# Optimization experiments

Measured on AMD Instinct MI355X. Metric: run time of the kernel, lower is better.

Reference implementation:

```python
import jax, jax.numpy as jnp
import numpy as np

B, D, H, NB = 4096, 2048, 2048, 4
BIN, BOUT = D // NB, H // NB
EPS = 1e-5


def _block_linear(x, W, b):
    # x: [B, nb*bin], W: [nb, bin, bout], b: [nb, bout] -> [B, nb*bout]
    xr = x.reshape(x.shape[0], NB, BIN)
    y = jnp.einsum('bni,nio->bno', xr, W) + b
    return y.reshape(x.shape[0], NB * BOUT)


def setup_inputs() -> dict:
    key = jax.random.key(0)
    ks = jax.random.split(key, 24)
    sW = 1.0 / np.sqrt(BIN)
    sR = 1.0 / np.sqrt(BOUT)
    inp = {
        'x': jax.random.normal(ks[0], (B, D), jnp.float32),
        'h_prev': jax.random.normal(ks[1], (B, H), jnp.float32),
        'c_prev': jax.random.normal(ks[2], (B, H), jnp.float32),
        'ln_g': jnp.ones((D,), jnp.float32),
        'ln_b': jnp.zeros((D,), jnp.float32),
        'conv_w': jax.random.normal(ks[3], (3,), jnp.float32) * 0.5,
        'conv_b': jnp.zeros((), jnp.float32),
    }
    names = ['Wz', 'Wi', 'Wf', 'Wo']
    for j, n in enumerate(names):
        inp[n] = jax.random.normal(ks[4 + j], (NB, BIN, BOUT), jnp.float32) * sW
        inp['b' + n[1]] = jax.random.normal(ks[8 + j], (NB, BOUT), jnp.float32) * sW
    rnames = ['Rz', 'Ri', 'Rf', 'Ro']
    for j, n in enumerate(rnames):
        inp[n] = jax.random.normal(ks[12 + j], (NB, BOUT, BOUT), jnp.float32) * sR
        inp['rb' + n[1]] = jax.random.normal(ks[16 + j], (NB, BOUT), jnp.float32) * sR
    return inp


def reference(x, h_prev, c_prev, ln_g, ln_b, conv_w, conv_b,
              Wz, bz, Wi, bi, Wf, bf, Wo, bo,
              Rz, rbz, Ri, rbi, Rf, rbf, Ro, rbo):
    # LayerNorm over the feature dim
    mu = jnp.mean(x, axis=-1, keepdims=True)
    var = jnp.mean((x - mu) ** 2, axis=-1, keepdims=True)
    x_norm = (x - mu) * jax.lax.rsqrt(var + EPS) * ln_g + ln_b

    # Causal conv1d (kernel 3) along the feature axis, then SiLU
    xp = jnp.pad(x_norm, ((0, 0), (2, 0)))  # left-pad 2 -> causal
    xc = conv_w[0] * xp[:, :D] + conv_w[1] * xp[:, 1:D + 1] + conv_w[2] * xp[:, 2:D + 2] + conv_b
    x_conv = jax.nn.silu(xc)

    z = jnp.tanh(_block_linear(x, Wz, bz) + _block_linear(h_prev, Rz, rbz))
    i = jax.nn.sigmoid(_block_linear(x_conv, Wi, bi) + _block_linear(h_prev, Ri, rbi))
    f = jax.nn.sigmoid(_block_linear(x_conv, Wf, bf) + _block_linear(h_prev, Rf, rbf))
    o = jax.nn.sigmoid(_block_linear(x, Wo, bo) + _block_linear(h_prev, Ro, rbo))

    c_t = f * c_prev + i * z
    h_t = o * jnp.tanh(c_t)
    return (h_t, c_t)
```

## Files before the change

kernel.cpp:

```cpp
#include <hip/hip_runtime.h>
#include <hip/hip_bf16.h>
#include <math.h>

#define BB 4096
#define DD 2048
#define HH 2048

typedef __bf16 bf16x8 __attribute__((ext_vector_type(8)));
typedef float f32x4 __attribute__((ext_vector_type(4)));

__device__ __forceinline__ void async16(const void* g, void* l) {
  __builtin_amdgcn_global_load_lds(
      (const __attribute__((address_space(1))) unsigned int*)g,
      (__attribute__((address_space(3))) unsigned int*)l,
      16, 0, 0);
}

__device__ __forceinline__ float sigmoidf_(float x) {
  return 1.0f / (1.0f + __expf(-x));
}
__device__ __forceinline__ float tanhf_(float x) {
  float t = __expf(-2.0f * fabsf(x));
  return copysignf((1.0f - t) / (1.0f + t), x);
}

__device__ __forceinline__ void store_bf8(__hip_bfloat16* dst, const float* v) {
  union { __hip_bfloat16 b[8]; uint4 u; } p;
#pragma unroll
  for (int e = 0; e < 8; e++) p.b[e] = __float2bfloat16(v[e]);
  *(uint4*)dst = p.u;
}

__global__ void prep_bias(const float* __restrict__ bz, const float* __restrict__ bi,
                          const float* __restrict__ bf, const float* __restrict__ bo,
                          const float* __restrict__ rbz, const float* __restrict__ rbi,
                          const float* __restrict__ rbf, const float* __restrict__ rbo,
                          float* __restrict__ bias) {
  int i = blockIdx.x * 256 + threadIdx.x;
  if (i < 2048) {
    bias[0 * 2048 + i] = bz[i] + rbz[i];
    bias[1 * 2048 + i] = bi[i] + rbi[i];
    bias[2 * 2048 + i] = bf[i] + rbf[i];
    bias[3 * 2048 + i] = bo[i] + rbo[i];
  }
}

__global__ __launch_bounds__(256) void prep_w(
    const float* __restrict__ Wz, const float* __restrict__ Wi,
    const float* __restrict__ Wf, const float* __restrict__ Wo,
    const float* __restrict__ Rz, const float* __restrict__ Ri,
    const float* __restrict__ Rf, const float* __restrict__ Ro,
    __hip_bfloat16* __restrict__ WT2) {
  const int jt = blockIdx.x;
  const int ksg = blockIdx.y;
  const int gn = blockIdx.z;
  const int g = gn >> 2, nn = gn & 3;
  const float* src;
  if (ksg < 4) src = (g == 0 ? Wz : g == 1 ? Wi : g == 2 ? Wf : Wo);
  else         src = (g == 0 ? Rz : g == 1 ? Ri : g == 2 ? Rf : Ro);
  const int t = threadIdx.x;
#pragma unroll
  for (int q = 0; q < 2; q++) {
    int u = t + q * 256;
    int ksl = u >> 7, j = (u >> 2) & 31, pc = u & 3;
    int c = pc ^ ((j >> 1) & 3);
    int kr = (ksg & 3) * 128 + ksl * 32 + c * 8;
    const float* s0 = src + ((size_t)nn * 512 + kr) * 512 + jt * 32 + j;
    float v[8];
#pragma unroll
    for (int e = 0; e < 8; e++) v[e] = s0[(size_t)e * 512];
    size_t gr = ((size_t)(gn * 16 + jt) * 32 + ksg * 4 + ksl) * 128 + j * 4 + pc;
    store_bf8(WT2 + gr * 8, v);
  }
}

__global__ __launch_bounds__(256) void prep_act(
    const float* __restrict__ x, const float* __restrict__ h,
    const float* __restrict__ lg, const float* __restrict__ lb,
    const float* __restrict__ cw, const float* __restrict__ cb,
    __hip_bfloat16* __restrict__ xh2, __hip_bfloat16* __restrict__ xc2) {
  const int r = blockIdx.x, t = threadIdx.x, l = t & 63;
  const int mb = r >> 7, rl = r & 127, swz = (rl >> 1) & 3;
  const int n = t >> 6, ktl = (t >> 2) & 15, pc = (t & 3) ^ swz;
  __shared__ float red[8];
  __shared__ float edge[256][2];
  const float* xr = x + (size_t)r * 2048;
  const float* hr = h + (size_t)r * 2048;
  float4 v0 = ((const float4*)xr)[t * 2];
  float4 v1 = ((const float4*)xr)[t * 2 + 1];
  float vv[8] = {v0.x, v0.y, v0.z, v0.w, v1.x, v1.y, v1.z, v1.w};
  float s = 0.f, s2 = 0.f;
#pragma unroll
  for (int e = 0; e < 8; e++) { s += vv[e]; s2 += vv[e] * vv[e]; }
#pragma unroll
  for (int off = 32; off > 0; off >>= 1) {
    s += __shfl_down(s, off);
    s2 += __shfl_down(s2, off);
  }
  const int w = t >> 6;
  if (l == 0) { red[w] = s; red[4 + w] = s2; }
  __syncthreads();
  const float mu = (red[0] + red[1] + red[2] + red[3]) * (1.0f / 2048.0f);
  const float var = (red[4] + red[5] + red[6] + red[7]) * (1.0f / 2048.0f) - mu * mu;
  const float rs = rsqrtf(var + 1e-5f);

  float4 h0 = ((const float4*)hr)[t * 2];
  float4 h1 = ((const float4*)hr)[t * 2 + 1];
  float hh[8] = {h0.x, h0.y, h0.z, h0.w, h1.x, h1.y, h1.z, h1.w};
  float4 g0 = ((const float4*)lg)[t * 2], g1 = ((const float4*)lg)[t * 2 + 1];
  float4 b0 = ((const float4*)lb)[t * 2], b1 = ((const float4*)lb)[t * 2 + 1];
  float gg[8] = {g0.x, g0.y, g0.z, g0.w, g1.x, g1.y, g1.z, g1.w};
  float bb[8] = {b0.x, b0.y, b0.z, b0.w, b1.x, b1.y, b1.z, b1.w};
  float fr[8];
#pragma unroll
  for (int e = 0; e < 8; e++) fr[e] = (vv[e] - mu) * rs * gg[e] + bb[e];

  const size_t bx = ((size_t)(mb * 4 + n) * 32 + ktl) * 512 + rl * 4 + pc;
  const size_t bh = ((size_t)(mb * 4 + n) * 32 + 16 + ktl) * 512 + rl * 4 + pc;
  store_bf8(xh2 + bx * 8, vv);
  store_bf8(xh2 + bh * 8, hh);

  edge[t][0] = fr[6]; edge[t][1] = fr[7];
  __syncthreads();
  float p6 = __shfl_up(fr[6], 1);
  float p7 = __shfl_up(fr[7], 1);
  if (l == 0) {
    p6 = (t > 0) ? edge[t - 1][0] : 0.f;
    p7 = (t > 0) ? edge[t - 1][1] : 0.f;
  }
  const float w0 = cw[0], w1 = cw[1], w2 = cw[2], cbv = cb[0];
  float sc[8];
  {
    float xc0 = w0 * p6 + w1 * p7 + w2 * fr[0] + cbv;
    float xc1 = w0 * p7 + w1 * fr[0] + w2 * fr[1] + cbv;
    sc[0] = xc0 * sigmoidf_(xc0);
    sc[1] = xc1 * sigmoidf_(xc1);
  }
#pragma unroll
  for (int e = 2; e < 8; e++) {
    float xc = w0 * fr[e - 2] + w1 * fr[e - 1] + w2 * fr[e] + cbv;
    sc[e] = xc * sigmoidf_(xc);
  }
  const size_t bc = ((size_t)(mb * 4 + n) * 16 + ktl) * 512 + rl * 4 + pc;
  store_bf8(xc2 + bc * 8, sc);
}

__global__ __launch_bounds__(512, 4) void gemm_fused(
    const __hip_bfloat16* __restrict__ xh2, const __hip_bfloat16* __restrict__ xc2,
    const __hip_bfloat16* __restrict__ WT2, const float* __restrict__ bias,
    const float* __restrict__ c_prev, float* __restrict__ out) {
  __shared__ __attribute__((aligned(16))) char smem[65536];
  __hip_bfloat16* zo = (__hip_bfloat16*)smem;

  const int mb = blockIdx.x, jt = blockIdx.y, n = blockIdx.z;
  const int t = threadIdx.x, w = t >> 6, l = t & 63;
  const int pair = w >> 2, mhalf = (w >> 1) & 1, jhalf = w & 1;
  const int lj = l & 15;

  const char* pA = (const char*)xh2 + (size_t)(mb * 4 + n) * 262144 + t * 16;
  const char* pC = (const char*)xc2 + (size_t)(mb * 4 + n) * 131072 + t * 16;
  const char* pB = (const char*)WT2 +
      (size_t)(n * 16 + jt * 2 + ((t >> 8) & 1)) * 65536 + ((t >> 7) & 1) * 2048 + (t & 127) * 16;
  char* dA = smem + t * 16;
  char* dB = smem + 32768 + t * 16;

  const int fo = lj * 64 + (((l >> 4) ^ ((lj >> 1) & 3)) * 16);
  const int g0 = pair ? 1 : 0, g1 = pair ? 2 : 3;

  f32x4 acc[4][2][2] = {};

  for (int ks2 = 0; ks2 < 16; ++ks2) {
    __syncthreads();
    async16(pA, dA);
    async16(pA + 8192, dA + 8192);
    if (ks2 < 8) {
      async16(pC, dA + 16384);
      async16(pC + 8192, dA + 24576);
    }
    async16(pB, dB);
    async16(pB + 4194304, dB + 8192);
    async16(pB + 8388608, dB + 16384);
    async16(pB + 12582912, dB + 24576);
    pA += 16384; pC += 16384; pB += 4096;
    __syncthreads();

    const char* Ab = ((ks2 < 8 && pair) ? smem + 16384 : smem) + mhalf * 4096 + fo;
    const char* Bb = smem + 32768 + jhalf * 4096 + fo;
#pragma unroll
    for (int kh = 0; kh < 2; ++kh) {
      bf16x8 af[4];
#pragma unroll
      for (int s = 0; s < 4; ++s)
        af[s] = *(const bf16x8*)(Ab + kh * 8192 + s * 1024);
#pragma unroll
      for (int sj = 0; sj < 2; ++sj) {
        bf16x8 b0 = *(const bf16x8*)(Bb + g0 * 8192 + kh * 2048 + sj * 1024);
        bf16x8 b1 = *(const bf16x8*)(Bb + g1 * 8192 + kh * 2048 + sj * 1024);
#pragma unroll
        for (int s = 0; s < 4; ++s) {
          acc[s][sj][0] = __builtin_amdgcn_mfma_f32_16x16x32_bf16(af[s], b0, acc[s][sj][0], 0, 0, 0);
          acc[s][sj][1] = __builtin_amdgcn_mfma_f32_16x16x32_bf16(af[s], b1, acc[s][sj][1], 0, 0, 0);
        }
      }
    }
  }

  const int r0 = (l >> 4) * 4;
  const int colb = n * 512 + jt * 64;
  __syncthreads();
  if (pair == 0) {
#pragma unroll
    for (int sj = 0; sj < 2; ++sj) {
      const int jc = jhalf * 32 + sj * 16 + lj;
      const float bz_ = bias[colb + jc];
      const float bo_ = bias[3 * 2048 + colb + jc];
#pragma unroll
      for (int s = 0; s < 4; ++s) {
#pragma unroll
        for (int rr = 0; rr < 4; ++rr) {
          const int rl = mhalf * 64 + s * 16 + r0 + rr;
          zo[rl * 72 + jc] = __float2bfloat16(tanhf_(acc[s][sj][0][rr] + bz_));
          zo[(128 + rl) * 72 + jc] = __float2bfloat16(sigmoidf_(acc[s][sj][1][rr] + bo_));
        }
      }
    }
  }
  __syncthreads();
  if (pair == 1) {
    const size_t HC = (size_t)BB * HH;
#pragma unroll
    for (int sj = 0; sj < 2; ++sj) {
      const int jc = jhalf * 32 + sj * 16 + lj;
      const int col = colb + jc;
      const float bi_ = bias[1 * 2048 + col];
      const float bf_ = bias[2 * 2048 + col];
#pragma unroll
      for (int s = 0; s < 4; ++s) {
#pragma unroll
        for (int rr = 0; rr < 4; ++rr) {
          const int rl = mhalf * 64 + s * 16 + r0 + rr;
          const int row = mb * 128 + rl;
          const float z  = __bfloat162float(zo[rl * 72 + jc]);
          const float og = __bfloat162float(zo[(128 + rl) * 72 + jc]);
          const float ig = sigmoidf_(acc[s][sj][0][rr] + bi_);
          const float fg = sigmoidf_(acc[s][sj][1][rr] + bf_);
          const float cp = c_prev[(size_t)row * 2048 + col];
          const float c = fg * cp + ig * z;
          const float hv = og * tanhf_(c);
          out[(size_t)row * 2048 + col] = hv;
          out[HC + (size_t)row * 2048 + col] = c;
        }
      }
    }
  }
}

extern "C" void kernel_launch(void* const* d_in, const int* in_sizes, int n_in,
                              void* d_out, int out_size, void* d_ws, size_t ws_size,
                              hipStream_t stream) {
  const float* x      = (const float*)d_in[0];
  const float* h_prev = (const float*)d_in[1];
  const float* c_prev = (const float*)d_in[2];
  const float* ln_g   = (const float*)d_in[3];
  const float* ln_b   = (const float*)d_in[4];
  const float* conv_w = (const float*)d_in[5];
  const float* conv_b = (const float*)d_in[6];
  const float* Wz = (const float*)d_in[7];
  const float* bz = (const float*)d_in[8];
  const float* Wi = (const float*)d_in[9];
  const float* bi = (const float*)d_in[10];
  const float* Wf = (const float*)d_in[11];
  const float* bf = (const float*)d_in[12];
  const float* Wo = (const float*)d_in[13];
  const float* bo = (const float*)d_in[14];
  const float* Rz = (const float*)d_in[15];
  const float* rbz = (const float*)d_in[16];
  const float* Ri = (const float*)d_in[17];
  const float* rbi = (const float*)d_in[18];
  const float* Rf = (const float*)d_in[19];
  const float* rbf = (const float*)d_in[20];
  const float* Ro = (const float*)d_in[21];
  const float* rbo = (const float*)d_in[22];
  float* out = (float*)d_out;

  char* ws = (char*)d_ws;
  __hip_bfloat16* xh2 = (__hip_bfloat16*)(ws);
  __hip_bfloat16* xc2 = (__hip_bfloat16*)(ws + 33554432);
  __hip_bfloat16* WT2 = (__hip_bfloat16*)(ws + 33554432 + 16777216);
  float* bias         = (float*)(ws + 33554432 + 2 * 16777216);

  prep_bias<<<8, 256, 0, stream>>>(bz, bi, bf, bo, rbz, rbi, rbf, rbo, bias);
  prep_w<<<dim3(16, 8, 16), 256, 0, stream>>>(Wz, Wi, Wf, Wo, Rz, Ri, Rf, Ro, WT2);
  prep_act<<<BB, 256, 0, stream>>>(x, h_prev, ln_g, ln_b, conv_w, conv_b, xh2, xc2);
  gemm_fused<<<dim3(32, 8, 4), 512, 0, stream>>>(xh2, xc2, WT2, bias, c_prev, out);
}
```

Baseline: 337.0 us.

## Double-buffer GEMM K loop with async LDS prefetch and remap block order

```diff
diff --git a/kernel.cpp b/kernel.cpp
--- a/kernel.cpp
+++ b/kernel.cpp
@@ -152,57 +152,76 @@
   __shared__ __attribute__((aligned(16))) char smem[65536];
   __hip_bfloat16* zo = (__hip_bfloat16*)smem;
 
-  const int mb = blockIdx.x, jt = blockIdx.y, n = blockIdx.z;
+  const int o = blockIdx.x;
+  const int lid = (o & 7) * 128 + (o >> 3);
+  const int mb = lid & 31, jt = (lid >> 5) & 7, n = lid >> 8;
+
   const int t = threadIdx.x, w = t >> 6, l = t & 63;
   const int pair = w >> 2, mhalf = (w >> 1) & 1, jhalf = w & 1;
   const int lj = l & 15;
 
   const char* pA = (const char*)xh2 + (size_t)(mb * 4 + n) * 262144 + t * 16;
   const char* pC = (const char*)xc2 + (size_t)(mb * 4 + n) * 131072 + t * 16;
+  const int bg = t >> 7, br = t & 127;
   const char* pB = (const char*)WT2 +
-      (size_t)(n * 16 + jt * 2 + ((t >> 8) & 1)) * 65536 + ((t >> 7) & 1) * 2048 + (t & 127) * 16;
-  char* dA = smem + t * 16;
-  char* dB = smem + 32768 + t * 16;
+      ((size_t)((bg * 4 + n) * 16 + jt * 2)) * 65536 + br * 16;
+  const int dAo = t * 16;
+  const int dBo = 16384 + bg * 4096 + br * 16;
 
   const int fo = lj * 64 + (((l >> 4) ^ ((lj >> 1) & 3)) * 16);
   const int g0 = pair ? 1 : 0, g1 = pair ? 2 : 3;
 
   f32x4 acc[4][2][2] = {};
 
-  for (int ks2 = 0; ks2 < 16; ++ks2) {
-    __syncthreads();
-    async16(pA, dA);
-    async16(pA + 8192, dA + 8192);
-    if (ks2 < 8) {
-      async16(pC, dA + 16384);
-      async16(pC + 8192, dA + 24576);
+  {
+    char* nb = smem;
+    async16(pA, nb + dAo);
+    async16(pC, nb + 8192 + dAo);
+    async16(pB, nb + dBo);
+    async16(pB + 65536, nb + dBo + 2048);
+  }
+
+  for (int ks = 0; ks < 32; ++ks) {
+    const int nxt = ks + 1;
+    if (nxt < 16) {
+      char* nb = smem + (nxt & 1) * 32768;
+      async16(pA + (size_t)nxt * 8192, nb + dAo);
+      async16(pC + (size_t)nxt * 8192, nb + 8192 + dAo);
+      async16(pB + (size_t)nxt * 2048, nb + dBo);
+      async16(pB + (size_t)nxt * 2048 + 65536, nb + dBo + 2048);
+      asm volatile("s_waitcnt vmcnt(4)" ::: "memory");
+    } else if (nxt < 32) {
+      char* nb = smem + (nxt & 1) * 32768;
+      async16(pA + (size_t)nxt * 8192, nb + dAo);
+      async16(pB + (size_t)nxt * 2048, nb + dBo);
+      async16(pB + (size_t)nxt * 2048 + 65536, nb + dBo + 2048);
+      asm volatile("s_waitcnt vmcnt(3)" ::: "memory");
+    } else {
+      asm volatile("s_waitcnt vmcnt(0)" ::: "memory");
     }
-    async16(pB, dB);
-    async16(pB + 4194304, dB + 8192);
-    async16(pB + 8388608, dB + 16384);
-    async16(pB + 12582912, dB + 24576);
-    pA += 16384; pC += 16384; pB += 4096;
-    __syncthreads();
-
-    const char* Ab = ((ks2 < 8 && pair) ? smem + 16384 : smem) + mhalf * 4096 + fo;
-    const char* Bb = smem + 32768 + jhalf * 4096 + fo;
-#pragma unroll
-    for (int kh = 0; kh < 2; ++kh) {
-      bf16x8 af[4];
-#pragma unroll
-      for (int s = 0; s < 4; ++s)
-        af[s] = *(const bf16x8*)(Ab + kh * 8192 + s * 1024);
-#pragma unroll
-      for (int sj = 0; sj < 2; ++sj) {
-        bf16x8 b0 = *(const bf16x8*)(Bb + g0 * 8192 + kh * 2048 + sj * 1024);
-        bf16x8 b1 = *(const bf16x8*)(Bb + g1 * 8192 + kh * 2048 + sj * 1024);
-#pragma unroll
-        for (int s = 0; s < 4; ++s) {
-          acc[s][sj][0] = __builtin_amdgcn_mfma_f32_16x16x32_bf16(af[s], b0, acc[s][sj][0], 0, 0, 0);
-          acc[s][sj][1] = __builtin_amdgcn_mfma_f32_16x16x32_bf16(af[s], b1, acc[s][sj][1], 0, 0, 0);
-        }
+    __builtin_amdgcn_s_barrier();
+    __builtin_amdgcn_sched_barrier(0);
+
+    const char* cb = smem + (ks & 1) * 32768;
+    const char* Ab = ((ks < 16 && pair) ? cb + 8192 : cb) + mhalf * 4096 + fo;
+    const char* Bb = cb + 16384 + jhalf * 2048 + fo;
+    bf16x8 af[4];
+#pragma unroll
+    for (int s = 0; s < 4; ++s)
+      af[s] = *(const bf16x8*)(Ab + s * 1024);
+#pragma unroll
+    for (int sj = 0; sj < 2; ++sj) {
+      bf16x8 b0 = *(const bf16x8*)(Bb + g0 * 4096 + sj * 1024);
+      bf16x8 b1 = *(const bf16x8*)(Bb + g1 * 4096 + sj * 1024);
+#pragma unroll
+      for (int s = 0; s < 4; ++s) {
+        acc[s][sj][0] = __builtin_amdgcn_mfma_f32_16x16x32_bf16(af[s], b0, acc[s][sj][0], 0, 0, 0);
+        acc[s][sj][1] = __builtin_amdgcn_mfma_f32_16x16x32_bf16(af[s], b1, acc[s][sj][1], 0, 0, 0);
       }
     }
+    __builtin_amdgcn_sched_barrier(0);
+    __builtin_amdgcn_s_barrier();
+    __builtin_amdgcn_sched_barrier(0);
   }
 
   const int r0 = (l >> 4) * 4;
@@ -292,5 +311,5 @@
   prep_bias<<<8, 256, 0, stream>>>(bz, bi, bf, bo, rbz, rbi, rbf, rbo, bias);
   prep_w<<<dim3(16, 8, 16), 256, 0, stream>>>(Wz, Wi, Wf, Wo, Rz, Ri, Rf, Ro, WT2);
   prep_act<<<BB, 256, 0, stream>>>(x, h_prev, ln_g, ln_b, conv_w, conv_b, xh2, xc2);
-  gemm_fused<<<dim3(32, 8, 4), 512, 0, stream>>>(xh2, xc2, WT2, bias, c_prev, out);
-}
+  gemm_fused<<<1024, 512, 0, stream>>>(xh2, xc2, WT2, bias, c_prev, out);
+}
```

Result: no change. 332.1 us (-1.5%).

## Pipeline GEMM main loop with 4-stage LDS ring, direct A register loads, XCD-aware grid

Applied to the files above, without the earlier changes.

```diff
diff --git a/kernel.cpp b/kernel.cpp
--- a/kernel.cpp
+++ b/kernel.cpp
@@ -14,6 +14,11 @@
       (const __attribute__((address_space(1))) unsigned int*)g,
       (__attribute__((address_space(3))) unsigned int*)l,
       16, 0, 0);
+}
+
+template <int N>
+__device__ __forceinline__ void wait_vmcnt() {
+  asm volatile("s_waitcnt vmcnt(%0)" ::"n"(N) : "memory");
 }
 
 __device__ __forceinline__ float sigmoidf_(float x) {
@@ -145,65 +150,112 @@
   store_bf8(xc2 + bc * 8, sc);
 }
 
-__global__ __launch_bounds__(512, 4) void gemm_fused(
+__global__ __launch_bounds__(512, 2) void gemm_fused(
     const __hip_bfloat16* __restrict__ xh2, const __hip_bfloat16* __restrict__ xc2,
     const __hip_bfloat16* __restrict__ WT2, const float* __restrict__ bias,
     const float* __restrict__ c_prev, float* __restrict__ out) {
   __shared__ __attribute__((aligned(16))) char smem[65536];
   __hip_bfloat16* zo = (__hip_bfloat16*)smem;
 
-  const int mb = blockIdx.x, jt = blockIdx.y, n = blockIdx.z;
+  const int o = blockIdx.x;
+  const int xcd = o & 7, sfx = o >> 3;
+  const int n = xcd >> 1;
+  const int jt = (xcd & 1) * 4 + (sfx & 3);
+  const int mb = sfx >> 2;
+
   const int t = threadIdx.x, w = t >> 6, l = t & 63;
   const int pair = w >> 2, mhalf = (w >> 1) & 1, jhalf = w & 1;
   const int lj = l & 15;
 
-  const char* pA = (const char*)xh2 + (size_t)(mb * 4 + n) * 262144 + t * 16;
-  const char* pC = (const char*)xc2 + (size_t)(mb * 4 + n) * 131072 + t * 16;
-  const char* pB = (const char*)WT2 +
-      (size_t)(n * 16 + jt * 2 + ((t >> 8) & 1)) * 65536 + ((t >> 7) & 1) * 2048 + (t & 127) * 16;
-  char* dA = smem + t * 16;
-  char* dB = smem + 32768 + t * 16;
-
   const int fo = lj * 64 + (((l >> 4) ^ ((lj >> 1) & 3)) * 16);
   const int g0 = pair ? 1 : 0, g1 = pair ? 2 : 3;
 
+  const char* gAx = (const char*)xh2 + (size_t)(mb * 4 + n) * 262144 + mhalf * 4096 + fo;
+  const char* gAc = (const char*)xc2 + (size_t)(mb * 4 + n) * 131072 + mhalf * 4096 + fo;
+
+  const int u0 = t, u1 = t + 512;
+  const int bg0 = u0 >> 8, bj0 = (u0 >> 7) & 1, br0 = u0 & 127;
+  const int bg1 = u1 >> 8, bj1 = (u1 >> 7) & 1, br1 = u1 & 127;
+  const char* gB0 = (const char*)WT2 +
+      ((size_t)((bg0 * 4 + n) * 16 + jt * 2 + bj0)) * 65536 + br0 * 16;
+  const char* gB1 = (const char*)WT2 +
+      ((size_t)((bg1 * 4 + n) * 16 + jt * 2 + bj1)) * 65536 + br1 * 16;
+  const int dB0 = bg0 * 4096 + bj0 * 2048 + br0 * 16;
+  const int dB1 = bg1 * 4096 + bj1 * 2048 + br1 * 16;
+
   f32x4 acc[4][2][2] = {};
-
-  for (int ks2 = 0; ks2 < 16; ++ks2) {
-    __syncthreads();
-    async16(pA, dA);
-    async16(pA + 8192, dA + 8192);
-    if (ks2 < 8) {
-      async16(pC, dA + 16384);
-      async16(pC + 8192, dA + 24576);
-    }
-    async16(pB, dB);
-    async16(pB + 4194304, dB + 8192);
-    async16(pB + 8388608, dB + 16384);
-    async16(pB + 12582912, dB + 24576);
-    pA += 16384; pC += 16384; pB += 4096;
-    __syncthreads();
-
-    const char* Ab = ((ks2 < 8 && pair) ? smem + 16384 : smem) + mhalf * 4096 + fo;
-    const char* Bb = smem + 32768 + jhalf * 4096 + fo;
-#pragma unroll
-    for (int kh = 0; kh < 2; ++kh) {
-      bf16x8 af[4];
-#pragma unroll
-      for (int s = 0; s < 4; ++s)
-        af[s] = *(const bf16x8*)(Ab + kh * 8192 + s * 1024);
-#pragma unroll
-      for (int sj = 0; sj < 2; ++sj) {
-        bf16x8 b0 = *(const bf16x8*)(Bb + g0 * 8192 + kh * 2048 + sj * 1024);
-        bf16x8 b1 = *(const bf16x8*)(Bb + g1 * 8192 + kh * 2048 + sj * 1024);
-#pragma unroll
-        for (int s = 0; s < 4; ++s) {
-          acc[s][sj][0] = __builtin_amdgcn_mfma_f32_16x16x32_bf16(af[s], b0, acc[s][sj][0], 0, 0, 0);
-          acc[s][sj][1] = __builtin_amdgcn_mfma_f32_16x16x32_bf16(af[s], b1, acc[s][sj][1], 0, 0, 0);
-        }
-      }
-    }
-  }
+  bf16x8 afa0, afa1, afa2, afa3, afb0, afb1, afb2, afb3;
+
+#define BAR() __builtin_amdgcn_s_barrier()
+#define SBZ() __builtin_amdgcn_sched_barrier(0)
+
+#define APTR(h) ((((h) < 16) && pair) ? (gAc + (size_t)(h) * 8192) \
+                                      : (gAx + (size_t)(h) * 8192))
+
+#define LOADA(h, X)                                                            \
+  do { if ((h) < 32) {                                                         \
+    const char* ap_ = APTR(h);                                                 \
+    af##X##0 = *(const bf16x8*)(ap_);                                          \
+    af##X##1 = *(const bf16x8*)(ap_ + 1024);                                   \
+    af##X##2 = *(const bf16x8*)(ap_ + 2048);                                   \
+    af##X##3 = *(const bf16x8*)(ap_ + 3072);                                   \
+  } } while (0)
+
+#define STAGEB(h)                                                              \
+  do { if ((h) < 32) {                                                         \
+    char* d_ = smem + ((h) & 3) * 16384;                                       \
+    async16(gB0 + (size_t)(h) * 2048, d_ + dB0);                               \
+    async16(gB1 + (size_t)(h) * 2048, d_ + dB1);                               \
+  } } while (0)
+
+#define MFMA8(C, sj, B0, B1)                                                   \
+  do {                                                                         \
+    acc[0][sj][0] = __builtin_amdgcn_mfma_f32_16x16x32_bf16(af##C##0, B0, acc[0][sj][0], 0, 0, 0); \
+    acc[1][sj][0] = __builtin_amdgcn_mfma_f32_16x16x32_bf16(af##C##1, B0, acc[1][sj][0], 0, 0, 0); \
+    acc[2][sj][0] = __builtin_amdgcn_mfma_f32_16x16x32_bf16(af##C##2, B0, acc[2][sj][0], 0, 0, 0); \
+    acc[3][sj][0] = __builtin_amdgcn_mfma_f32_16x16x32_bf16(af##C##3, B0, acc[3][sj][0], 0, 0, 0); \
+    acc[0][sj][1] = __builtin_amdgcn_mfma_f32_16x16x32_bf16(af##C##0, B1, acc[0][sj][1], 0, 0, 0); \
+    acc[1][sj][1] = __builtin_amdgcn_mfma_f32_16x16x32_bf16(af##C##1, B1, acc[1][sj][1], 0, 0, 0); \
+    acc[2][sj][1] = __builtin_amdgcn_mfma_f32_16x16x32_bf16(af##C##2, B1, acc[2][sj][1], 0, 0, 0); \
+    acc[3][sj][1] = __builtin_amdgcn_mfma_f32_16x16x32_bf16(af##C##3, B1, acc[3][sj][1], 0, 0, 0); \
+  } while (0)
+
+#define HALF(h, C, X)                                                          \
+  do {                                                                         \
+    const char* Bb_ = smem + ((h) & 3) * 16384 + jhalf * 2048 + fo;            \
+    bf16x8 b00 = *(const bf16x8*)(Bb_ + g0 * 4096);                            \
+    bf16x8 b10 = *(const bf16x8*)(Bb_ + g1 * 4096);                            \
+    bf16x8 b01 = *(const bf16x8*)(Bb_ + g0 * 4096 + 1024);                     \
+    bf16x8 b11 = *(const bf16x8*)(Bb_ + g1 * 4096 + 1024);                     \
+    LOADA((h) + 1, X);                                                         \
+    STAGEB((h) + 3);                                                           \
+    SBZ();                                                                     \
+    __builtin_amdgcn_s_setprio(1);                                             \
+    MFMA8(C, 0, b00, b10);                                                     \
+    MFMA8(C, 1, b01, b11);                                                     \
+    __builtin_amdgcn_s_setprio(0);                                             \
+    SBZ();                                                                     \
+    if ((h) < 31) {                                                            \
+      wait_vmcnt<8>();                                                         \
+      BAR(); SBZ();                                                            \
+    }                                                                          \
+  } while (0)
+
+  LOADA(0, a);
+  STAGEB(0);
+  STAGEB(1);
+  STAGEB(2);
+  wait_vmcnt<4>();
+  BAR(); SBZ();
+
+  HALF(0, a, b);  HALF(1, b, a);  HALF(2, a, b);  HALF(3, b, a);
+  HALF(4, a, b);  HALF(5, b, a);  HALF(6, a, b);  HALF(7, b, a);
+  HALF(8, a, b);  HALF(9, b, a);  HALF(10, a, b); HALF(11, b, a);
+  HALF(12, a, b); HALF(13, b, a); HALF(14, a, b); HALF(15, b, a);
+  HALF(16, a, b); HALF(17, b, a); HALF(18, a, b); HALF(19, b, a);
+  HALF(20, a, b); HALF(21, b, a); HALF(22, a, b); HALF(23, b, a);
+  HALF(24, a, b); HALF(25, b, a); HALF(26, a, b); HALF(27, b, a);
+  HALF(28, a, b); HALF(29, b, a); HALF(30, a, b); HALF(31, b, a);
 
   const int r0 = (l >> 4) * 4;
   const int colb = n * 512 + jt * 64;
@@ -292,5 +344,5 @@
   prep_bias<<<8, 256, 0, stream>>>(bz, bi, bf, bo, rbz, rbi, rbf, rbo, bias);
   prep_w<<<dim3(16, 8, 16), 256, 0, stream>>>(Wz, Wi, Wf, Wo, Rz, Ri, Rf, Ro, WT2);
   prep_act<<<BB, 256, 0, stream>>>(x, h_prev, ln_g, ln_b, conv_w, conv_b, xh2, xc2);
-  gemm_fused<<<dim3(32, 8, 4), 512, 0, stream>>>(xh2, xc2, WT2, bias, c_prev, out);
-}
+  gemm_fused<<<1024, 512, 0, stream>>>(xh2, xc2, WT2, bias, c_prev, out);
+}
```

New measurement: 346.2 us. 2.7% more time.

## Merge prep kernels into one launch and stage weight transpose through LDS

Applied to the files above, without the earlier changes.

```diff
diff --git a/kernel.cpp b/kernel.cpp
--- a/kernel.cpp
+++ b/kernel.cpp
@@ -31,118 +31,134 @@
   *(uint4*)dst = p.u;
 }
 
-__global__ void prep_bias(const float* __restrict__ bz, const float* __restrict__ bi,
-                          const float* __restrict__ bf, const float* __restrict__ bo,
-                          const float* __restrict__ rbz, const float* __restrict__ rbi,
-                          const float* __restrict__ rbf, const float* __restrict__ rbo,
-                          float* __restrict__ bias) {
-  int i = blockIdx.x * 256 + threadIdx.x;
-  if (i < 2048) {
-    bias[0 * 2048 + i] = bz[i] + rbz[i];
-    bias[1 * 2048 + i] = bi[i] + rbi[i];
-    bias[2 * 2048 + i] = bf[i] + rbf[i];
-    bias[3 * 2048 + i] = bo[i] + rbo[i];
-  }
-}
-
-__global__ __launch_bounds__(256) void prep_w(
+__global__ __launch_bounds__(256) void prep_all(
+    const float* __restrict__ x, const float* __restrict__ h,
+    const float* __restrict__ lg, const float* __restrict__ lb,
+    const float* __restrict__ cw, const float* __restrict__ cb,
+    __hip_bfloat16* __restrict__ xh2, __hip_bfloat16* __restrict__ xc2,
     const float* __restrict__ Wz, const float* __restrict__ Wi,
     const float* __restrict__ Wf, const float* __restrict__ Wo,
     const float* __restrict__ Rz, const float* __restrict__ Ri,
     const float* __restrict__ Rf, const float* __restrict__ Ro,
-    __hip_bfloat16* __restrict__ WT2) {
-  const int jt = blockIdx.x;
-  const int ksg = blockIdx.y;
-  const int gn = blockIdx.z;
-  const int g = gn >> 2, nn = gn & 3;
-  const float* src;
-  if (ksg < 4) src = (g == 0 ? Wz : g == 1 ? Wi : g == 2 ? Wf : Wo);
-  else         src = (g == 0 ? Rz : g == 1 ? Ri : g == 2 ? Rf : Ro);
-  const int t = threadIdx.x;
-#pragma unroll
-  for (int q = 0; q < 2; q++) {
-    int u = t + q * 256;
-    int ksl = u >> 7, j = (u >> 2) & 31, pc = u & 3;
-    int c = pc ^ ((j >> 1) & 3);
-    int kr = (ksg & 3) * 128 + ksl * 32 + c * 8;
-    const float* s0 = src + ((size_t)nn * 512 + kr) * 512 + jt * 32 + j;
-    float v[8];
-#pragma unroll
-    for (int e = 0; e < 8; e++) v[e] = s0[(size_t)e * 512];
-    size_t gr = ((size_t)(gn * 16 + jt) * 32 + ksg * 4 + ksl) * 128 + j * 4 + pc;
-    store_bf8(WT2 + gr * 8, v);
+    __hip_bfloat16* __restrict__ WT2,
+    const float* __restrict__ bz, const float* __restrict__ bi,
+    const float* __restrict__ bf, const float* __restrict__ bo,
+    const float* __restrict__ rbz, const float* __restrict__ rbi,
+    const float* __restrict__ rbf, const float* __restrict__ rbo,
+    float* __restrict__ bias) {
+  __shared__ float smf[4224];
+  const int b = blockIdx.x, t = threadIdx.x;
+
+  if (b < 4096) {
+    const int r = b, l = t & 63;
+    const int mb = r >> 7, rl = r & 127, swz = (rl >> 1) & 3;
+    const int n = t >> 6, ktl = (t >> 2) & 15, pc = (t & 3) ^ swz;
+    float* red = smf;
+    float* edge = smf + 8;
+    const float* xr = x + (size_t)r * 2048;
+    const float* hr = h + (size_t)r * 2048;
+    float4 v0 = ((const float4*)xr)[t * 2];
+    float4 v1 = ((const float4*)xr)[t * 2 + 1];
+    float vv[8] = {v0.x, v0.y, v0.z, v0.w, v1.x, v1.y, v1.z, v1.w};
+    float s = 0.f, s2 = 0.f;
+#pragma unroll
+    for (int e = 0; e < 8; e++) { s += vv[e]; s2 += vv[e] * vv[e]; }
+#pragma unroll
+    for (int off = 32; off > 0; off >>= 1) {
+      s += __shfl_down(s, off);
+      s2 += __shfl_down(s2, off);
+    }
+    const int w = t >> 6;
+    if (l == 0) { red[w] = s; red[4 + w] = s2; }
+    __syncthreads();
+    const float mu = (red[0] + red[1] + red[2] + red[3]) * (1.0f / 2048.0f);
+    const float var = (red[4] + red[5] + red[6] + red[7]) * (1.0f / 2048.0f) - mu * mu;
+    const float rs = rsqrtf(var + 1e-5f);
+
+    float4 h0 = ((const float4*)hr)[t * 2];
+    float4 h1 = ((const float4*)hr)[t * 2 + 1];
+    float hh[8] = {h0.x, h0.y, h0.z, h0.w, h1.x, h1.y, h1.z, h1.w};
+    float4 g0 = ((const float4*)lg)[t * 2], g1 = ((const float4*)lg)[t * 2 + 1];
+    float4 b0 = ((const float4*)lb)[t * 2], b1 = ((const float4*)lb)[t * 2 + 1];
+    float gg[8] = {g0.x, g0.y, g0.z, g0.w, g1.x, g1.y, g1.z, g1.w};
+    float bbv[8] = {b0.x, b0.y, b0.z, b0.w, b1.x, b1.y, b1.z, b1.w};
+    float fr[8];
+#pragma unroll
+    for (int e = 0; e < 8; e++) fr[e] = (vv[e] - mu) * rs * gg[e] + bbv[e];
+
+    const size_t bx = ((size_t)(mb * 4 + n) * 32 + ktl) * 512 + rl * 4 + pc;
+    const size_t bh = ((size_t)(mb * 4 + n) * 32 + 16 + ktl) * 512 + rl * 4 + pc;
+    store_bf8(xh2 + bx * 8, vv);
+    store_bf8(xh2 + bh * 8, hh);
+
+    edge[t * 2 + 0] = fr[6]; edge[t * 2 + 1] = fr[7];
+    __syncthreads();
+    float p6 = __shfl_up(fr[6], 1);
+    float p7 = __shfl_up(fr[7], 1);
+    if (l == 0) {
+      p6 = (t > 0) ? edge[(t - 1) * 2 + 0] : 0.f;
+      p7 = (t > 0) ? edge[(t - 1) * 2 + 1] : 0.f;
+    }
+    const float w0 = cw[0], w1 = cw[1], w2 = cw[2], cbv = cb[0];
+    float sc[8];
+    {
+      float xc0 = w0 * p6 + w1 * p7 + w2 * fr[0] + cbv;
+      float xc1 = w0 * p7 + w1 * fr[0] + w2 * fr[1] + cbv;
+      sc[0] = xc0 * sigmoidf_(xc0);
+      sc[1] = xc1 * sigmoidf_(xc1);
+    }
+#pragma unroll
+    for (int e = 2; e < 8; e++) {
+      float xc = w0 * fr[e - 2] + w1 * fr[e - 1] + w2 * fr[e] + cbv;
+      sc[e] = xc * sigmoidf_(xc);
+    }
+    const size_t bc = ((size_t)(mb * 4 + n) * 16 + ktl) * 512 + rl * 4 + pc;
+    store_bf8(xc2 + bc * 8, sc);
+
+  } else if (b < 6144) {
+    const int flat = b - 4096;
+    const int jt = flat & 15;
+    const int ksg = (flat >> 4) & 7;
+    const int gn = flat >> 7;
+    const int g = gn >> 2, nn = gn & 3;
+    const float* src;
+    if (ksg < 4) src = (g == 0 ? Wz : g == 1 ? Wi : g == 2 ? Wf : Wo);
+    else         src = (g == 0 ? Rz : g == 1 ? Ri : g == 2 ? Rf : Ro);
+    const int kb = (ksg & 3) * 128;
+
+    {
+      const int r8 = t >> 3, c4 = t & 7;
+      const float* sp = src + ((size_t)nn * 512 + kb + r8) * 512 + jt * 32 + c4 * 4;
+#pragma unroll
+      for (int rr = 0; rr < 4; rr++) {
+        float4 v = *(const float4*)(sp + (size_t)rr * 32 * 512);
+        float* d = smf + (r8 + rr * 32) * 33 + c4 * 4;
+        d[0] = v.x; d[1] = v.y; d[2] = v.z; d[3] = v.w;
+      }
+    }
+    __syncthreads();
+#pragma unroll
+    for (int q = 0; q < 2; q++) {
+      int u = t + q * 256;
+      int ksl = u >> 7, j = (u >> 2) & 31, pc = u & 3;
+      int c = pc ^ ((j >> 1) & 3);
+      int krl = ksl * 32 + c * 8;
+      float v[8];
+#pragma unroll
+      for (int e = 0; e < 8; e++) v[e] = smf[(krl + e) * 33 + j];
+      size_t gr = ((size_t)(gn * 16 + jt) * 32 + ksg * 4 + ksl) * 128 + j * 4 + pc;
+      store_bf8(WT2 + gr * 8, v);
+    }
+
+  } else {
+    int i = (b - 6144) * 256 + t;
+    if (i < 2048) {
+      bias[0 * 2048 + i] = bz[i] + rbz[i];
+      bias[1 * 2048 + i] = bi[i] + rbi[i];
+      bias[2 * 2048 + i] = bf[i] + rbf[i];
+      bias[3 * 2048 + i] = bo[i] + rbo[i];
+    }
   }
-}
-
-__global__ __launch_bounds__(256) void prep_act(
-    const float* __restrict__ x, const float* __restrict__ h,
-    const float* __restrict__ lg, const float* __restrict__ lb,
-    const float* __restrict__ cw, const float* __restrict__ cb,
-    __hip_bfloat16* __restrict__ xh2, __hip_bfloat16* __restrict__ xc2) {
-  const int r = blockIdx.x, t = threadIdx.x, l = t & 63;
-  const int mb = r >> 7, rl = r & 127, swz = (rl >> 1) & 3;
-  const int n = t >> 6, ktl = (t >> 2) & 15, pc = (t & 3) ^ swz;
-  __shared__ float red[8];
-  __shared__ float edge[256][2];
-  const float* xr = x + (size_t)r * 2048;
-  const float* hr = h + (size_t)r * 2048;
-  float4 v0 = ((const float4*)xr)[t * 2];
-  float4 v1 = ((const float4*)xr)[t * 2 + 1];
-  float vv[8] = {v0.x, v0.y, v0.z, v0.w, v1.x, v1.y, v1.z, v1.w};
-  float s = 0.f, s2 = 0.f;
-#pragma unroll
-  for (int e = 0; e < 8; e++) { s += vv[e]; s2 += vv[e] * vv[e]; }
-#pragma unroll
-  for (int off = 32; off > 0; off >>= 1) {
-    s += __shfl_down(s, off);
-    s2 += __shfl_down(s2, off);
-  }
-  const int w = t >> 6;
-  if (l == 0) { red[w] = s; red[4 + w] = s2; }
-  __syncthreads();
-  const float mu = (red[0] + red[1] + red[2] + red[3]) * (1.0f / 2048.0f);
-  const float var = (red[4] + red[5] + red[6] + red[7]) * (1.0f / 2048.0f) - mu * mu;
-  const float rs = rsqrtf(var + 1e-5f);
-
-  float4 h0 = ((const float4*)hr)[t * 2];
-  float4 h1 = ((const float4*)hr)[t * 2 + 1];
-  float hh[8] = {h0.x, h0.y, h0.z, h0.w, h1.x, h1.y, h1.z, h1.w};
-  float4 g0 = ((const float4*)lg)[t * 2], g1 = ((const float4*)lg)[t * 2 + 1];
-  float4 b0 = ((const float4*)lb)[t * 2], b1 = ((const float4*)lb)[t * 2 + 1];
-  float gg[8] = {g0.x, g0.y, g0.z, g0.w, g1.x, g1.y, g1.z, g1.w};
-  float bb[8] = {b0.x, b0.y, b0.z, b0.w, b1.x, b1.y, b1.z, b1.w};
-  float fr[8];
-#pragma unroll
-  for (int e = 0; e < 8; e++) fr[e] = (vv[e] - mu) * rs * gg[e] + bb[e];
-
-  const size_t bx = ((size_t)(mb * 4 + n) * 32 + ktl) * 512 + rl * 4 + pc;
-  const size_t bh = ((size_t)(mb * 4 + n) * 32 + 16 + ktl) * 512 + rl * 4 + pc;
-  store_bf8(xh2 + bx * 8, vv);
-  store_bf8(xh2 + bh * 8, hh);
-
-  edge[t][0] = fr[6]; edge[t][1] = fr[7];
-  __syncthreads();
-  float p6 = __shfl_up(fr[6], 1);
-  float p7 = __shfl_up(fr[7], 1);
-  if (l == 0) {
-    p6 = (t > 0) ? edge[t - 1][0] : 0.f;
-    p7 = (t > 0) ? edge[t - 1][1] : 0.f;
-  }
-  const float w0 = cw[0], w1 = cw[1], w2 = cw[2], cbv = cb[0];
-  float sc[8];
-  {
-    float xc0 = w0 * p6 + w1 * p7 + w2 * fr[0] + cbv;
-    float xc1 = w0 * p7 + w1 * fr[0] + w2 * fr[1] + cbv;
-    sc[0] = xc0 * sigmoidf_(xc0);
-    sc[1] = xc1 * sigmoidf_(xc1);
-  }
-#pragma unroll
-  for (int e = 2; e < 8; e++) {
-    float xc = w0 * fr[e - 2] + w1 * fr[e - 1] + w2 * fr[e] + cbv;
-    sc[e] = xc * sigmoidf_(xc);
-  }
-  const size_t bc = ((size_t)(mb * 4 + n) * 16 + ktl) * 512 + rl * 4 + pc;
-  store_bf8(xc2 + bc * 8, sc);
 }
 
 __global__ __launch_bounds__(512, 4) void gemm_fused(
@@ -289,8 +305,9 @@
   __hip_bfloat16* WT2 = (__hip_bfloat16*)(ws + 33554432 + 16777216);
   float* bias         = (float*)(ws + 33554432 + 2 * 16777216);
 
-  prep_bias<<<8, 256, 0, stream>>>(bz, bi, bf, bo, rbz, rbi, rbf, rbo, bias);
-  prep_w<<<dim3(16, 8, 16), 256, 0, stream>>>(Wz, Wi, Wf, Wo, Rz, Ri, Rf, Ro, WT2);
-  prep_act<<<BB, 256, 0, stream>>>(x, h_prev, ln_g, ln_b, conv_w, conv_b, xh2, xc2);
+  prep_all<<<6152, 256, 0, stream>>>(
+      x, h_prev, ln_g, ln_b, conv_w, conv_b, xh2, xc2,
+      Wz, Wi, Wf, Wo, Rz, Ri, Rf, Ro, WT2,
+      bz, bi, bf, bo, rbz, rbi, rbf, rbo, bias);
   gemm_fused<<<dim3(32, 8, 4), 512, 0, stream>>>(xh2, xc2, WT2, bias, c_prev, out);
 }
```

After: 321.8 us. 4.5% less time.
